# Kernel tuning notes

Hardware: AMD Instinct MI355X
Metric: run time of the kernel (lower is better)

Reference implementation:

```python
import jax, jax.numpy as jnp
import numpy as np

N = 10000
E = 160000
UNITS = 64
NUM_RBF = 32
CUTOFF = 1.0


def _xavier(k, shape):
    fan_out, fan_in = shape
    lim = float(np.sqrt(6.0 / (fan_in + fan_out)))
    return jax.random.uniform(k, shape, minval=-lim, maxval=lim, dtype=jnp.float32)


def setup_inputs() -> dict:
    key = jax.random.key(0)
    ks = jax.random.split(key, 16)
    inp = {
        "edge_index": jax.random.randint(ks[0], (2, E), 0, N),
        "edge_weight": jax.random.uniform(ks[1], (E,), dtype=jnp.float32),
        "edge_attr": jax.random.normal(ks[2], (E, NUM_RBF), dtype=jnp.float32),
        "X": jax.random.normal(ks[3], (N, UNITS, 3, 3), dtype=jnp.float32),
        # scalar MLP: num_rbf -> units -> 2*units -> 3*units
        "Ws0": _xavier(ks[4], (UNITS, NUM_RBF)), "bs0": jnp.zeros((UNITS,), jnp.float32),
        "Ws1": _xavier(ks[5], (2 * UNITS, UNITS)), "bs1": jnp.zeros((2 * UNITS,), jnp.float32),
        "Ws2": _xavier(ks[6], (3 * UNITS, 2 * UNITS)), "bs2": jnp.zeros((3 * UNITS,), jnp.float32),
    }
    for i in range(6):
        inp[f"Wt{i}"] = _xavier(ks[7 + i], (UNITS, UNITS))
    return inp


def cosine_cutoff(r, cutoff):
    return jnp.where(r < cutoff, 0.5 * (jnp.cos(jnp.pi * r / cutoff) + 1.0), 0.0)


def tensor_norm(X):
    # X: [N, units, 3, 3] -> [N, units]
    return jnp.sum(X * X, axis=(-2, -1))


def decompose_tensor(X):
    eye = jnp.eye(3, dtype=X.dtype)
    trace = jnp.trace(X, axis1=-2, axis2=-1)  # [N, units]
    I = (trace / 3.0)[..., None, None] * eye
    A = 0.5 * (X - jnp.swapaxes(X, -2, -1))
    S = 0.5 * (X + jnp.swapaxes(X, -2, -1)) - I
    return I, A, S


def channel_linear(T, W):
    # linear over the channel dim: [N, c, 3, 3] x [d, c] -> [N, d, 3, 3]
    return jnp.einsum('ncij,dc->ndij', T, W)


def reference(edge_index, edge_weight, edge_attr, X,
              Ws0, bs0, Ws1, bs1, Ws2, bs2,
              Wt0, Wt1, Wt2, Wt3, Wt4, Wt5):
    act = jax.nn.silu
    C = cosine_cutoff(edge_weight, CUTOFF)  # [E]
    h = act(edge_attr @ Ws0.T + bs0)
    h = act(h @ Ws1.T + bs1)
    h = act(h @ Ws2.T + bs2)  # [E, 3*units]
    ea = (h * C[:, None]).reshape(h.shape[0], UNITS, 3)  # [E, units, 3]

    X = X / (tensor_norm(X) + 1.0)[..., None, None]
    I, A, S = decompose_tensor(X)
    I = channel_linear(I, Wt0)
    A = channel_linear(A, Wt1)
    S = channel_linear(S, Wt2)
    Y = I + A + S

    src, dst = edge_index[0], edge_index[1]
    n = X.shape[0]
    # message = per-edge radial scaling of gathered node tensors; aggregate at src
    Im = jax.ops.segment_sum(ea[..., 0, None, None] * I[dst], src, num_segments=n)
    Am = jax.ops.segment_sum(ea[..., 1, None, None] * A[dst], src, num_segments=n)
    Sm = jax.ops.segment_sum(ea[..., 2, None, None] * S[dst], src, num_segments=n)
    msg = Im + Am + Sm

    # O(3): symmetrized product of batched 3x3 matmuls
    AB = jnp.matmul(msg, Y) + jnp.matmul(Y, msg)
    I2, A2, S2 = decompose_tensor(AB)
    normp1 = (tensor_norm(I2 + A2 + S2) + 1.0)[..., None, None]
    I2 = channel_linear(I2 / normp1, Wt3)
    A2 = channel_linear(A2 / normp1, Wt4)
    S2 = channel_linear(S2 / normp1, Wt5)
    dX = I2 + A2 + S2
    return X + dX + jnp.matmul(dX, dX)
```

## Files before the change

kernel.cpp:

```cpp
#include <hip/hip_runtime.h>
#include <math.h>

#define NN 10000
#define EE 160000

#define OFF_WTT 0
#define OFF_PK  24576
#define OFF_B2P 41984
#define OFF_IASH 42176
#define OFF_EAH 3242176
#define OFF_ATTRP 18602176
#define OFF_CP  21162176
#define OFF_INT 21322176

typedef __attribute__((ext_vector_type(8))) _Float16 h16x8;
typedef __attribute__((ext_vector_type(2))) __fp16 fp16x2_raw;
typedef __attribute__((ext_vector_type(4))) float f32x4;

__device__ __forceinline__ float silu_f(float x) {
    return x * __builtin_amdgcn_rcpf(1.0f + __expf(-x));
}
__device__ __forceinline__ unsigned int pkh(float a, float b) {
    union { fp16x2_raw h; unsigned int u; } cv;
    cv.h = __builtin_amdgcn_cvt_pkrtz(a, b);
    return cv.u;
}
__device__ __forceinline__ unsigned short f2h(float f) {
    union { _Float16 h; unsigned short u; } cv; cv.h = (_Float16)f; return cv.u;
}
__device__ __forceinline__ float h2f(unsigned short s) {
    union { unsigned short u; _Float16 h; } cv; cv.u = s; return (float)cv.h;
}
__device__ __forceinline__ float h2f_lo(unsigned int u) { return h2f((unsigned short)(u & 0xffffu)); }
__device__ __forceinline__ float h2f_hi(unsigned int u) { return h2f((unsigned short)(u >> 16)); }
__device__ __forceinline__ unsigned int bperm(int addr, unsigned int v) {
    return (unsigned int)__builtin_amdgcn_ds_bpermute(addr, (int)v);
}

__global__ void k_prep(const float* __restrict__ Wt0, const float* __restrict__ Wt1,
                       const float* __restrict__ Wt2, const float* __restrict__ Wt3,
                       const float* __restrict__ Wt4, const float* __restrict__ Wt5,
                       const float* __restrict__ Ws0, const float* __restrict__ Ws1,
                       const float* __restrict__ Ws2, const float* __restrict__ bs2,
                       const int* __restrict__ ei,
                       float* __restrict__ WtT, unsigned short* __restrict__ PK,
                       float* __restrict__ bs2p, int* __restrict__ counts) {
    int idx = blockIdx.x * 256 + threadIdx.x;
    if (idx < 24576) {
        int k = idx >> 12, r = idx & 4095;
        int c = r >> 6, d = r & 63;
        const float* W = (k == 0) ? Wt0 : (k == 1) ? Wt1 : (k == 2) ? Wt2
                       : (k == 3) ? Wt3 : (k == 4) ? Wt4 : Wt5;
        WtT[idx] = W[d * 64 + c];
    } else if (idx < 26624) {
        int q = idx - 24576;
        int ot = q >> 9, r = q & 511, lane = r >> 3, j = r & 7;
        int k = ((lane >> 4) * 8) + j, o = ot * 16 + (lane & 15);
        PK[q] = f2h(Ws0[o * 32 + k]);
    } else if (idx < 34816) {
        int q = idx - 24576;
        int i = q - 2048, ch = i >> 9, r = i & 511, lane = r >> 3, j = r & 7;
        int ot = ch >> 1, ks = ch & 1;
        int k = ks * 32 + (lane >> 4) * 8 + j, o = ot * 16 + (lane & 15);
        PK[q] = f2h(Ws1[o * 64 + k]);
    } else if (idx < 59392) {
        int q = idx - 24576;
        int i = q - 10240, ch = i >> 9, r = i & 511, lane = r >> 3, j = r & 7;
        int ot = ch >> 2, ks = ch & 3;
        int k = ks * 32 + (lane >> 4) * 8 + j;
        int op = ot * 16 + (lane & 15);
        int o = (op & 63) * 3 + (op >> 6);
        PK[q] = f2h(Ws2[o * 128 + k]);
    } else if (idx < 59584) {
        int op = idx - 59392;
        bs2p[op] = bs2[(op & 63) * 3 + (op >> 6)];
    } else if (idx < 59584 + EE) {
        int e = idx - 59584;
        atomicAdd(&counts[ei[e]], 1);
    }
}

__global__ __launch_bounds__(256) void k_scan(const int* __restrict__ counts,
                                              int* __restrict__ offsets) {
    __shared__ int sums[256];
    int t = threadIdx.x;
    int base = t * 40;
    int s = 0;
    if (base < NN) {
        const int4* p = (const int4*)(counts + base);
#pragma unroll
        for (int q = 0; q < 10; ++q) { int4 a = p[q]; s += a.x + a.y + a.z + a.w; }
    }
    sums[t] = s;
    __syncthreads();
    for (int off = 1; off < 256; off <<= 1) {
        int tmp = (t >= off) ? sums[t - off] : 0;
        __syncthreads();
        sums[t] += tmp;
        __syncthreads();
    }
    int run = sums[t] - s;
    if (base < NN) {
        const int4* p = (const int4*)(counts + base);
#pragma unroll
        for (int q = 0; q < 10; ++q) {
            int4 a = p[q];
            offsets[base + 4 * q + 0] = run; run += a.x;
            offsets[base + 4 * q + 1] = run; run += a.y;
            offsets[base + 4 * q + 2] = run; run += a.z;
            offsets[base + 4 * q + 3] = run; run += a.w;
        }
    }
    if (t == 255) offsets[NN] = run;
}

__global__ void k_fill(const int* __restrict__ ei, const int* __restrict__ offsets,
                       const float* __restrict__ attr, const float* __restrict__ ew,
                       int* __restrict__ cursor, int* __restrict__ dstp,
                       unsigned short* __restrict__ attrP, float* __restrict__ Cp) {
    int e = blockIdx.x * 256 + threadIdx.x;
    if (e < EE) {
        int s = ei[e];
        int pos = offsets[s] + atomicAdd(&cursor[s], 1);
        dstp[pos] = ei[EE + e];
        const float4* ap = (const float4*)(attr + (size_t)e * 32);
        unsigned int pk[16];
#pragma unroll
        for (int q = 0; q < 8; ++q) {
            float4 v = ap[q];
            pk[2 * q]     = pkh(v.x, v.y);
            pk[2 * q + 1] = pkh(v.z, v.w);
        }
        uint4* dst = (uint4*)(attrP + (size_t)pos * 32);
#pragma unroll
        for (int q = 0; q < 4; ++q)
            dst[q] = make_uint4(pk[4 * q], pk[4 * q + 1], pk[4 * q + 2], pk[4 * q + 3]);
        float rw = ew[e];
        Cp[pos] = (rw < 1.0f) ? 0.5f * (cosf(3.14159265358979f * rw) + 1.0f) : 0.0f;
    }
}

__global__ __launch_bounds__(256) void k_mlpnp(const unsigned short* __restrict__ attrP,
                                               const float* __restrict__ Cp,
                                               const unsigned short* __restrict__ PK,
                                               const float* __restrict__ bs0,
                                               const float* __restrict__ bs1,
                                               const float* __restrict__ bs2p,
                                               const float* __restrict__ X,
                                               const float* __restrict__ WtT,
                                               unsigned short* __restrict__ eah,
                                               unsigned int* __restrict__ IASu) {
    __shared__ float SH[4][1344];
    int t = threadIdx.x, w = t >> 6, l = t & 63;
    if (blockIdx.x < EE / 64) {
        int e = l & 15, lg = l >> 4;
        int pos = blockIdx.x * 64 + w * 16 + e;
        const h16x8* P1 = (const h16x8*)PK;
        const h16x8* P2 = (const h16x8*)(PK + 2048);
        const h16x8* P3 = (const h16x8*)(PK + 10240);
        union U8 { h16x8 h; unsigned int u[4]; uint4 v; };
        U8 B1;
        B1.v = *((const uint4*)(attrP + (size_t)pos * 32) + lg);
        float C = Cp[pos];
        int src0 = ((lg & 1) * 32 + e) * 4;
        int src1 = src0 + 64;
        bool hi = (lg >= 2);

        unsigned int h01[8], h23[8];
#pragma unroll
        for (int ot = 0; ot < 4; ++ot) {
            float4 bb = *(const float4*)&bs0[ot * 16 + lg * 4];
            f32x4 acc = {bb.x, bb.y, bb.z, bb.w};
            acc = __builtin_amdgcn_mfma_f32_16x16x32_f16(P1[ot * 64 + l], B1.h, acc, 0, 0, 0);
            h01[ot] = pkh(silu_f(acc[0]), silu_f(acc[1]));
            h23[ot] = pkh(silu_f(acc[2]), silu_f(acc[3]));
        }
        U8 B2a, B2b;
        {
            unsigned int a, b;
            a = bperm(src0, h01[0]); b = bperm(src0, h01[1]); B2a.u[0] = hi ? b : a;
            a = bperm(src0, h23[0]); b = bperm(src0, h23[1]); B2a.u[1] = hi ? b : a;
            a = bperm(src1, h01[0]); b = bperm(src1, h01[1]); B2a.u[2] = hi ? b : a;
            a = bperm(src1, h23[0]); b = bperm(src1, h23[1]); B2a.u[3] = hi ? b : a;
            a = bperm(src0, h01[2]); b = bperm(src0, h01[3]); B2b.u[0] = hi ? b : a;
            a = bperm(src0, h23[2]); b = bperm(src0, h23[3]); B2b.u[1] = hi ? b : a;
            a = bperm(src1, h01[2]); b = bperm(src1, h01[3]); B2b.u[2] = hi ? b : a;
            a = bperm(src1, h23[2]); b = bperm(src1, h23[3]); B2b.u[3] = hi ? b : a;
        }
#pragma unroll
        for (int ot = 0; ot < 8; ++ot) {
            float4 bb = *(const float4*)&bs1[ot * 16 + lg * 4];
            f32x4 acc = {bb.x, bb.y, bb.z, bb.w};
            acc = __builtin_amdgcn_mfma_f32_16x16x32_f16(P2[(ot * 2 + 0) * 64 + l], B2a.h, acc, 0, 0, 0);
            acc = __builtin_amdgcn_mfma_f32_16x16x32_f16(P2[(ot * 2 + 1) * 64 + l], B2b.h, acc, 0, 0, 0);
            h01[ot] = pkh(silu_f(acc[0]), silu_f(acc[1]));
            h23[ot] = pkh(silu_f(acc[2]), silu_f(acc[3]));
        }
        U8 B3[4];
#pragma unroll
        for (int ks = 0; ks < 4; ++ks) {
            unsigned int a, b;
            a = bperm(src0, h01[ks * 2]); b = bperm(src0, h01[ks * 2 + 1]); B3[ks].u[0] = hi ? b : a;
            a = bperm(src0, h23[ks * 2]); b = bperm(src0, h23[ks * 2 + 1]); B3[ks].u[1] = hi ? b : a;
            a = bperm(src1, h01[ks * 2]); b = bperm(src1, h01[ks * 2 + 1]); B3[ks].u[2] = hi ? b : a;
            a = bperm(src1, h23[ks * 2]); b = bperm(src1, h23[ks * 2 + 1]); B3[ks].u[3] = hi ? b : a;
        }
        size_t ebase = (size_t)pos * 192;
#pragma unroll
        for (int ot = 0; ot < 12; ++ot) {
            float4 bb = *(const float4*)&bs2p[ot * 16 + lg * 4];
            f32x4 acc = {bb.x, bb.y, bb.z, bb.w};
            acc = __builtin_amdgcn_mfma_f32_16x16x32_f16(P3[(ot * 4 + 0) * 64 + l], B3[0].h, acc, 0, 0, 0);
            acc = __builtin_amdgcn_mfma_f32_16x16x32_f16(P3[(ot * 4 + 1) * 64 + l], B3[1].h, acc, 0, 0, 0);
            acc = __builtin_amdgcn_mfma_f32_16x16x32_f16(P3[(ot * 4 + 2) * 64 + l], B3[2].h, acc, 0, 0, 0);
            acc = __builtin_amdgcn_mfma_f32_16x16x32_f16(P3[(ot * 4 + 3) * 64 + l], B3[3].h, acc, 0, 0, 0);
            unsigned int u01 = pkh(silu_f(acc[0]) * C, silu_f(acc[1]) * C);
            unsigned int u23 = pkh(silu_f(acc[2]) * C, silu_f(acc[3]) * C);
            *(uint2*)&eah[ebase + ot * 16 + lg * 4] = make_uint2(u01, u23);
        }
    } else {
        int c = l;
        int n = (blockIdx.x - EE / 64) * 4 + w;
        float* xs = SH[w];
        float (*L12)[12] = (float (*)[12])(xs + 576);
#pragma unroll
        for (int i = 0; i < 9; i++) xs[c + 64 * i] = X[(size_t)n * 576 + c + 64 * i];
        __builtin_amdgcn_wave_barrier();
        float x[9];
#pragma unroll
        for (int j = 0; j < 9; j++) x[j] = xs[c * 9 + j];
        float nrm = 0.f;
#pragma unroll
        for (int j = 0; j < 9; j++) nrm += x[j] * x[j];
        float inv = __builtin_amdgcn_rcpf(nrm + 1.0f);
#pragma unroll
        for (int j = 0; j < 9; j++) x[j] *= inv;
        float tr3 = (x[0] + x[4] + x[8]) * (1.0f / 3.0f);
        L12[c][0] = tr3;
        L12[c][1] = 0.5f * (x[1] - x[3]);
        L12[c][2] = 0.5f * (x[2] - x[6]);
        L12[c][3] = 0.5f * (x[5] - x[7]);
        L12[c][4] = x[0] - tr3;
        L12[c][5] = x[4] - tr3;
        L12[c][6] = 0.5f * (x[1] + x[3]);
        L12[c][7] = 0.5f * (x[2] + x[6]);
        L12[c][8] = 0.5f * (x[5] + x[7]);
        __builtin_amdgcn_wave_barrier();
        int d = c;
        const float* W0 = WtT;
        const float* W1 = WtT + 4096;
        const float* W2 = WtT + 8192;
        float aI = 0, aA0 = 0, aA1 = 0, aA2 = 0, aS0 = 0, aS1 = 0, aS2 = 0, aS3 = 0, aS4 = 0;
        for (int cc = 0; cc < 64; ++cc) {
            float w0 = W0[cc * 64 + d], w1 = W1[cc * 64 + d], w2 = W2[cc * 64 + d];
            float4 L0 = *(const float4*)&L12[cc][0];
            float4 L1 = *(const float4*)&L12[cc][4];
            float L8 = L12[cc][8];
            aI  += w0 * L0.x;
            aA0 += w1 * L0.y; aA1 += w1 * L0.z; aA2 += w1 * L0.w;
            aS0 += w2 * L1.x; aS1 += w2 * L1.y; aS2 += w2 * L1.z;
            aS3 += w2 * L1.w; aS4 += w2 * L8;
        }
        unsigned int* op = IASu + (size_t)n * 320 + d;
        op[0]   = pkh(aI, aA0);
        op[64]  = pkh(aA1, aA2);
        op[128] = pkh(aS0, aS1);
        op[192] = pkh(aS2, aS3);
        op[256] = pkh(aS4, 0.0f);
    }
}

__global__ __launch_bounds__(256) void k_aggout(const int* __restrict__ offsets,
                                                const int* __restrict__ dstp,
                                                const unsigned short* __restrict__ eah,
                                                const unsigned int* __restrict__ IASu,
                                                const float* __restrict__ X,
                                                const float* __restrict__ WtT,
                                                float* __restrict__ out) {
    int t = threadIdx.x, w = t >> 6, c = t & 63;
    int n = blockIdx.x * 4 + w;
    __shared__ float XS[4][576];
    __shared__ float LO[4][768];
    float* xs = XS[w];
    float* lo = LO[w];
#pragma unroll
    for (int i = 0; i < 9; i++) xs[c + 64 * i] = X[(size_t)n * 576 + c + 64 * i];

    int beg = offsets[n], end = offsets[n + 1];
    int dv = 0;
    { int idx = beg + c; if (idx < end) dv = dstp[idx]; }
    float m0 = 0, m1 = 0, m2 = 0, m3 = 0, m4 = 0, m5 = 0, m6 = 0, m7 = 0, m8 = 0;
    int i = beg;
    for (; i + 4 <= end; i += 4) {
        int q0 = i - beg;
        int d0 = (q0 < 64)     ? __shfl(dv, q0)     : dstp[i];
        int d1 = (q0 + 1 < 64) ? __shfl(dv, q0 + 1) : dstp[i + 1];
        int d2 = (q0 + 2 < 64) ? __shfl(dv, q0 + 2) : dstp[i + 2];
        int d3 = (q0 + 3 < 64) ? __shfl(dv, q0 + 3) : dstp[i + 3];
        int dd[4] = {d0, d1, d2, d3};
        float a[4][3];
        unsigned int u[4][5];
#pragma unroll
        for (int q = 0; q < 4; ++q) {
            const unsigned short* ep = eah + (size_t)(i + q) * 192;
            a[q][0] = h2f(ep[c]); a[q][1] = h2f(ep[64 + c]); a[q][2] = h2f(ep[128 + c]);
            const unsigned int* p = IASu + (size_t)dd[q] * 320 + c;
            u[q][0] = p[0]; u[q][1] = p[64]; u[q][2] = p[128]; u[q][3] = p[192]; u[q][4] = p[256];
        }
#pragma unroll
        for (int q = 0; q < 4; ++q) {
            m0 += a[q][0] * h2f_lo(u[q][0]); m1 += a[q][1] * h2f_hi(u[q][0]);
            m2 += a[q][1] * h2f_lo(u[q][1]); m3 += a[q][1] * h2f_hi(u[q][1]);
            m4 += a[q][2] * h2f_lo(u[q][2]); m5 += a[q][2] * h2f_hi(u[q][2]);
            m6 += a[q][2] * h2f_lo(u[q][3]); m7 += a[q][2] * h2f_hi(u[q][3]);
            m8 += a[q][2] * h2f_lo(u[q][4]);
        }
    }
    for (; i < end; ++i) {
        int q0 = i - beg;
        int dst = (q0 < 64) ? __shfl(dv, q0) : dstp[i];
        const unsigned short* ep = eah + (size_t)i * 192;
        float a0 = h2f(ep[c]), a1 = h2f(ep[64 + c]), a2 = h2f(ep[128 + c]);
        const unsigned int* p = IASu + (size_t)dst * 320 + c;
        unsigned int u0 = p[0], u1 = p[64], u2 = p[128], u3 = p[192], u4 = p[256];
        m0 += a0 * h2f_lo(u0); m1 += a1 * h2f_hi(u0);
        m2 += a1 * h2f_lo(u1); m3 += a1 * h2f_hi(u1);
        m4 += a2 * h2f_lo(u2); m5 += a2 * h2f_hi(u2);
        m6 += a2 * h2f_lo(u3); m7 += a2 * h2f_hi(u3);
        m8 += a2 * h2f_lo(u4);
    }
    const unsigned int* yp = IASu + (size_t)n * 320 + c;
    unsigned int y0 = yp[0], y1 = yp[64], y2 = yp[128], y3 = yp[192], y4 = yp[256];
    float yI = h2f_lo(y0), yA0 = h2f_hi(y0), yA1 = h2f_lo(y1), yA2 = h2f_hi(y1);
    float yS0 = h2f_lo(y2), yS1 = h2f_hi(y2), yS2 = h2f_lo(y3), yS3 = h2f_hi(y3);
    float yS4 = h2f_lo(y4);

    float M[3][3] = {
        { m0 + m4,   m1 + m6,  m2 + m7 },
        { -m1 + m6,  m0 + m5,  m3 + m8 },
        { -m2 + m7, -m3 + m8,  m0 - m4 - m5 } };
    float Y[3][3] = {
        { yI + yS0,   yA0 + yS2,  yA1 + yS3 },
        { -yA0 + yS2, yI + yS1,   yA2 + yS4 },
        { -yA1 + yS3, -yA2 + yS4, yI - yS0 - yS1 } };
    float AB[3][3];
#pragma unroll
    for (int ii = 0; ii < 3; ii++)
#pragma unroll
        for (int j = 0; j < 3; j++) {
            float s = 0.f;
#pragma unroll
            for (int k = 0; k < 3; k++) s += M[ii][k] * Y[k][j] + Y[ii][k] * M[k][j];
            AB[ii][j] = s;
        }
    float tr3 = (AB[0][0] + AB[1][1] + AB[2][2]) * (1.0f / 3.0f);
    float fro = 0.f;
#pragma unroll
    for (int ii = 0; ii < 3; ii++)
#pragma unroll
        for (int j = 0; j < 3; j++) fro += AB[ii][j] * AB[ii][j];
    float inv = __builtin_amdgcn_rcpf(fro + 1.0f);
    float (*L12)[12] = (float (*)[12])lo;
    L12[c][0] = tr3 * inv;
    L12[c][1] = 0.5f * (AB[0][1] - AB[1][0]) * inv;
    L12[c][2] = 0.5f * (AB[0][2] - AB[2][0]) * inv;
    L12[c][3] = 0.5f * (AB[1][2] - AB[2][1]) * inv;
    L12[c][4] = (AB[0][0] - tr3) * inv;
    L12[c][5] = (AB[1][1] - tr3) * inv;
    L12[c][6] = 0.5f * (AB[0][1] + AB[1][0]) * inv;
    L12[c][7] = 0.5f * (AB[0][2] + AB[2][0]) * inv;
    L12[c][8] = 0.5f * (AB[1][2] + AB[2][1]) * inv;
    __builtin_amdgcn_wave_barrier();
    int d = c;
    const float* W3 = WtT + 3 * 4096;
    const float* W4 = WtT + 4 * 4096;
    const float* W5 = WtT + 5 * 4096;
    float aI = 0, aA0 = 0, aA1 = 0, aA2 = 0, aS0 = 0, aS1 = 0, aS2 = 0, aS3 = 0, aS4 = 0;
    for (int cc = 0; cc < 64; ++cc) {
        float w3 = W3[cc * 64 + d], w4 = W4[cc * 64 + d], w5 = W5[cc * 64 + d];
        float4 L0 = *(const float4*)&L12[cc][0];
        float4 L1 = *(const float4*)&L12[cc][4];
        float L8 = L12[cc][8];
        aI  += w3 * L0.x;
        aA0 += w4 * L0.y; aA1 += w4 * L0.z; aA2 += w4 * L0.w;
        aS0 += w5 * L1.x; aS1 += w5 * L1.y; aS2 += w5 * L1.z;
        aS3 += w5 * L1.w; aS4 += w5 * L8;
    }
    float dX[3][3] = {
        { aI + aS0,   aA0 + aS2,  aA1 + aS3 },
        { -aA0 + aS2, aI + aS1,   aA2 + aS4 },
        { -aA1 + aS3, -aA2 + aS4, aI - aS0 - aS1 } };
    float D2[3][3];
#pragma unroll
    for (int ii = 0; ii < 3; ii++)
#pragma unroll
        for (int j = 0; j < 3; j++) {
            float s = 0.f;
#pragma unroll
            for (int k = 0; k < 3; k++) s += dX[ii][k] * dX[k][j];
            D2[ii][j] = s;
        }
    float x[9];
    __builtin_amdgcn_wave_barrier();
#pragma unroll
    for (int j = 0; j < 9; j++) x[j] = xs[d * 9 + j];
    float nrm = 0.f;
#pragma unroll
    for (int j = 0; j < 9; j++) nrm += x[j] * x[j];
    float xinv = __builtin_amdgcn_rcpf(nrm + 1.0f);
    __builtin_amdgcn_wave_barrier();
#pragma unroll
    for (int ii = 0; ii < 3; ii++)
#pragma unroll
        for (int j = 0; j < 3; j++)
            lo[d * 9 + ii * 3 + j] = x[ii * 3 + j] * xinv + dX[ii][j] + D2[ii][j];
    __builtin_amdgcn_wave_barrier();
#pragma unroll
    for (int ii = 0; ii < 9; ii++) out[(size_t)n * 576 + c + 64 * ii] = lo[c + 64 * ii];
}

extern "C" void kernel_launch(void* const* d_in, const int* in_sizes, int n_in,
                              void* d_out, int out_size, void* d_ws, size_t ws_size,
                              hipStream_t stream) {
    (void)in_sizes; (void)n_in; (void)out_size; (void)ws_size;
    const int* ei = (const int*)d_in[0];
    const float* ew = (const float*)d_in[1];
    const float* attr = (const float*)d_in[2];
    const float* X = (const float*)d_in[3];
    const float* Ws0 = (const float*)d_in[4];
    const float* bs0 = (const float*)d_in[5];
    const float* Ws1 = (const float*)d_in[6];
    const float* bs1 = (const float*)d_in[7];
    const float* Ws2 = (const float*)d_in[8];
    const float* bs2 = (const float*)d_in[9];
    const float* Wt0 = (const float*)d_in[10];
    const float* Wt1 = (const float*)d_in[11];
    const float* Wt2 = (const float*)d_in[12];
    const float* Wt3 = (const float*)d_in[13];
    const float* Wt4 = (const float*)d_in[14];
    const float* Wt5 = (const float*)d_in[15];
    float* ws = (float*)d_ws;
    int* ibase = (int*)(ws + OFF_INT);
    int* counts = ibase;
    int* cursor = ibase + NN;
    int* offsets = ibase + 2 * NN;
    int* dstp = ibase + 3 * NN + 1;
    unsigned short* PK = (unsigned short*)(ws + OFF_PK);
    unsigned int* IASu = (unsigned int*)(ws + OFF_IASH);
    unsigned short* eah = (unsigned short*)(ws + OFF_EAH);
    unsigned short* attrP = (unsigned short*)(ws + OFF_ATTRP);
    float* Cp = ws + OFF_CP;

    (void)hipMemsetAsync(counts, 0, 2 * NN * sizeof(int), stream);
    k_prep<<<(59584 + EE + 255) / 256, 256, 0, stream>>>(
        Wt0, Wt1, Wt2, Wt3, Wt4, Wt5, Ws0, Ws1, Ws2, bs2, ei,
        ws, PK, ws + OFF_B2P, counts);
    k_scan<<<1, 256, 0, stream>>>(counts, offsets);
    k_fill<<<(EE + 255) / 256, 256, 0, stream>>>(ei, offsets, attr, ew, cursor, dstp, attrP, Cp);
    k_mlpnp<<<EE / 64 + NN / 4, 256, 0, stream>>>(attrP, Cp, PK, bs0, bs1, ws + OFF_B2P,
                                                  X, ws, eah, IASu);
    k_aggout<<<NN / 4, 256, 0, stream>>>(offsets, dstp, eah, IASu, X, ws, (float*)d_out);
}
```

Baseline: 160.9 us.

## Regroup kernels: fuse node prep into fill, stage MLP weights in LDS, split aggregation

Node-side tensor preparation moves from the MLP kernel into the fill kernel. The edge MLP becomes its own kernel that stages the layer-2/3 fp16 weights (64KB) in shared memory and processes 256 edges per block across four iterations, instead of reading the weights from global memory for each 64-edge block. The aggregation kernel now assigns two waves per node, each summing half of the edge range, and merges the partial sums through shared memory. This aims to cut repeated weight fetches and shorten per-node serial loops, at the cost of 64KB LDS per block (lower occupancy), an extra block barrier, and dropping the shuffle-based dst prefetch.

New measurement: 165.1 us. +2.6%, slower.

```diff
diff --git a/kernel.cpp b/kernel.cpp
--- a/kernel.cpp
+++ b/kernel.cpp
@@ -114,12 +114,21 @@
     if (t == 255) offsets[NN] = run;
 }
 
-__global__ void k_fill(const int* __restrict__ ei, const int* __restrict__ offsets,
-                       const float* __restrict__ attr, const float* __restrict__ ew,
-                       int* __restrict__ cursor, int* __restrict__ dstp,
-                       unsigned short* __restrict__ attrP, float* __restrict__ Cp) {
-    int e = blockIdx.x * 256 + threadIdx.x;
-    if (e < EE) {
+__global__ __launch_bounds__(256) void k_fillnp(const int* __restrict__ ei,
+                                                const int* __restrict__ offsets,
+                                                const float* __restrict__ attr,
+                                                const float* __restrict__ ew,
+                                                const float* __restrict__ X,
+                                                const float* __restrict__ WtT,
+                                                int* __restrict__ cursor,
+                                                int* __restrict__ dstp,
+                                                unsigned short* __restrict__ attrP,
+                                                float* __restrict__ Cp,
+                                                unsigned int* __restrict__ IASu) {
+    __shared__ float SH[4][1344];
+    int t = threadIdx.x, w = t >> 6, l = t & 63;
+    if (blockIdx.x < 625) {
+        int e = blockIdx.x * 256 + t;
         int s = ei[e];
         int pos = offsets[s] + atomicAdd(&cursor[s], 1);
         dstp[pos] = ei[EE + e];
@@ -137,90 +146,9 @@
             dst[q] = make_uint4(pk[4 * q], pk[4 * q + 1], pk[4 * q + 2], pk[4 * q + 3]);
         float rw = ew[e];
         Cp[pos] = (rw < 1.0f) ? 0.5f * (cosf(3.14159265358979f * rw) + 1.0f) : 0.0f;
-    }
-}
-
-__global__ __launch_bounds__(256) void k_mlpnp(const unsigned short* __restrict__ attrP,
-                                               const float* __restrict__ Cp,
-                                               const unsigned short* __restrict__ PK,
-                                               const float* __restrict__ bs0,
-                                               const float* __restrict__ bs1,
-                                               const float* __restrict__ bs2p,
-                                               const float* __restrict__ X,
-                                               const float* __restrict__ WtT,
-                                               unsigned short* __restrict__ eah,
-                                               unsigned int* __restrict__ IASu) {
-    __shared__ float SH[4][1344];
-    int t = threadIdx.x, w = t >> 6, l = t & 63;
-    if (blockIdx.x < EE / 64) {
-        int e = l & 15, lg = l >> 4;
-        int pos = blockIdx.x * 64 + w * 16 + e;
-        const h16x8* P1 = (const h16x8*)PK;
-        const h16x8* P2 = (const h16x8*)(PK + 2048);
-        const h16x8* P3 = (const h16x8*)(PK + 10240);
-        union U8 { h16x8 h; unsigned int u[4]; uint4 v; };
-        U8 B1;
-        B1.v = *((const uint4*)(attrP + (size_t)pos * 32) + lg);
-        float C = Cp[pos];
-        int src0 = ((lg & 1) * 32 + e) * 4;
-        int src1 = src0 + 64;
-        bool hi = (lg >= 2);
-
-        unsigned int h01[8], h23[8];
-#pragma unroll
-        for (int ot = 0; ot < 4; ++ot) {
-            float4 bb = *(const float4*)&bs0[ot * 16 + lg * 4];
-            f32x4 acc = {bb.x, bb.y, bb.z, bb.w};
-            acc = __builtin_amdgcn_mfma_f32_16x16x32_f16(P1[ot * 64 + l], B1.h, acc, 0, 0, 0);
-            h01[ot] = pkh(silu_f(acc[0]), silu_f(acc[1]));
-            h23[ot] = pkh(silu_f(acc[2]), silu_f(acc[3]));
-        }
-        U8 B2a, B2b;
-        {
-            unsigned int a, b;
-            a = bperm(src0, h01[0]); b = bperm(src0, h01[1]); B2a.u[0] = hi ? b : a;
-            a = bperm(src0, h23[0]); b = bperm(src0, h23[1]); B2a.u[1] = hi ? b : a;
-            a = bperm(src1, h01[0]); b = bperm(src1, h01[1]); B2a.u[2] = hi ? b : a;
-            a = bperm(src1, h23[0]); b = bperm(src1, h23[1]); B2a.u[3] = hi ? b : a;
-            a = bperm(src0, h01[2]); b = bperm(src0, h01[3]); B2b.u[0] = hi ? b : a;
-            a = bperm(src0, h23[2]); b = bperm(src0, h23[3]); B2b.u[1] = hi ? b : a;
-            a = bperm(src1, h01[2]); b = bperm(src1, h01[3]); B2b.u[2] = hi ? b : a;
-            a = bperm(src1, h23[2]); b = bperm(src1, h23[3]); B2b.u[3] = hi ? b : a;
-        }
-#pragma unroll
-        for (int ot = 0; ot < 8; ++ot) {
-            float4 bb = *(const float4*)&bs1[ot * 16 + lg * 4];
-            f32x4 acc = {bb.x, bb.y, bb.z, bb.w};
-            acc = __builtin_amdgcn_mfma_f32_16x16x32_f16(P2[(ot * 2 + 0) * 64 + l], B2a.h, acc, 0, 0, 0);
-            acc = __builtin_amdgcn_mfma_f32_16x16x32_f16(P2[(ot * 2 + 1) * 64 + l], B2b.h, acc, 0, 0, 0);
-            h01[ot] = pkh(silu_f(acc[0]), silu_f(acc[1]));
-            h23[ot] = pkh(silu_f(acc[2]), silu_f(acc[3]));
-        }
-        U8 B3[4];
-#pragma unroll
-        for (int ks = 0; ks < 4; ++ks) {
-            unsigned int a, b;
-            a = bperm(src0, h01[ks * 2]); b = bperm(src0, h01[ks * 2 + 1]); B3[ks].u[0] = hi ? b : a;
-            a = bperm(src0, h23[ks * 2]); b = bperm(src0, h23[ks * 2 + 1]); B3[ks].u[1] = hi ? b : a;
-            a = bperm(src1, h01[ks * 2]); b = bperm(src1, h01[ks * 2 + 1]); B3[ks].u[2] = hi ? b : a;
-            a = bperm(src1, h23[ks * 2]); b = bperm(src1, h23[ks * 2 + 1]); B3[ks].u[3] = hi ? b : a;
-        }
-        size_t ebase = (size_t)pos * 192;
-#pragma unroll
-        for (int ot = 0; ot < 12; ++ot) {
-            float4 bb = *(const float4*)&bs2p[ot * 16 + lg * 4];
-            f32x4 acc = {bb.x, bb.y, bb.z, bb.w};
-            acc = __builtin_amdgcn_mfma_f32_16x16x32_f16(P3[(ot * 4 + 0) * 64 + l], B3[0].h, acc, 0, 0, 0);
-            acc = __builtin_amdgcn_mfma_f32_16x16x32_f16(P3[(ot * 4 + 1) * 64 + l], B3[1].h, acc, 0, 0, 0);
-            acc = __builtin_amdgcn_mfma_f32_16x16x32_f16(P3[(ot * 4 + 2) * 64 + l], B3[2].h, acc, 0, 0, 0);
-            acc = __builtin_amdgcn_mfma_f32_16x16x32_f16(P3[(ot * 4 + 3) * 64 + l], B3[3].h, acc, 0, 0, 0);
-            unsigned int u01 = pkh(silu_f(acc[0]) * C, silu_f(acc[1]) * C);
-            unsigned int u23 = pkh(silu_f(acc[2]) * C, silu_f(acc[3]) * C);
-            *(uint2*)&eah[ebase + ot * 16 + lg * 4] = make_uint2(u01, u23);
-        }
     } else {
         int c = l;
-        int n = (blockIdx.x - EE / 64) * 4 + w;
+        int n = (blockIdx.x - 625) * 4 + w;
         float* xs = SH[w];
         float (*L12)[12] = (float (*)[12])(xs + 576);
 #pragma unroll
@@ -270,6 +198,92 @@
     }
 }
 
+__global__ __launch_bounds__(256) void k_mlp(const unsigned short* __restrict__ attrP,
+                                             const float* __restrict__ Cp,
+                                             const unsigned short* __restrict__ PK,
+                                             const float* __restrict__ bs0,
+                                             const float* __restrict__ bs1,
+                                             const float* __restrict__ bs2p,
+                                             unsigned short* __restrict__ eah) {
+    __shared__ unsigned short WL[32768];
+    int t = threadIdx.x, w = t >> 6, l = t & 63;
+    {
+        const uint4* src = (const uint4*)(PK + 2048);
+        uint4* dst = (uint4*)WL;
+#pragma unroll
+        for (int q = 0; q < 16; ++q) dst[t + q * 256] = src[t + q * 256];
+    }
+    __syncthreads();
+    int e = l & 15, lg = l >> 4;
+    const h16x8* P1 = (const h16x8*)PK;
+    const h16x8* P2 = (const h16x8*)WL;
+    const h16x8* P3 = (const h16x8*)(WL + 8192);
+    int src0 = ((lg & 1) * 32 + e) * 4;
+    int src1 = src0 + 64;
+    bool hi = (lg >= 2);
+
+    for (int it = 0; it < 4; ++it) {
+        int pos = blockIdx.x * 256 + w * 64 + it * 16 + e;
+        union U8 { h16x8 h; unsigned int u[4]; uint4 v; };
+        U8 B1;
+        B1.v = *((const uint4*)(attrP + (size_t)pos * 32) + lg);
+        float C = Cp[pos];
+
+        unsigned int h01[8], h23[8];
+#pragma unroll
+        for (int ot = 0; ot < 4; ++ot) {
+            float4 bb = *(const float4*)&bs0[ot * 16 + lg * 4];
+            f32x4 acc = {bb.x, bb.y, bb.z, bb.w};
+            acc = __builtin_amdgcn_mfma_f32_16x16x32_f16(P1[ot * 64 + l], B1.h, acc, 0, 0, 0);
+            h01[ot] = pkh(silu_f(acc[0]), silu_f(acc[1]));
+            h23[ot] = pkh(silu_f(acc[2]), silu_f(acc[3]));
+        }
+        U8 B2a, B2b;
+        {
+            unsigned int a, b;
+            a = bperm(src0, h01[0]); b = bperm(src0, h01[1]); B2a.u[0] = hi ? b : a;
+            a = bperm(src0, h23[0]); b = bperm(src0, h23[1]); B2a.u[1] = hi ? b : a;
+            a = bperm(src1, h01[0]); b = bperm(src1, h01[1]); B2a.u[2] = hi ? b : a;
+            a = bperm(src1, h23[0]); b = bperm(src1, h23[1]); B2a.u[3] = hi ? b : a;
+            a = bperm(src0, h01[2]); b = bperm(src0, h01[3]); B2b.u[0] = hi ? b : a;
+            a = bperm(src0, h23[2]); b = bperm(src0, h23[3]); B2b.u[1] = hi ? b : a;
+            a = bperm(src1, h01[2]); b = bperm(src1, h01[3]); B2b.u[2] = hi ? b : a;
+            a = bperm(src1, h23[2]); b = bperm(src1, h23[3]); B2b.u[3] = hi ? b : a;
+        }
+#pragma unroll
+        for (int ot = 0; ot < 8; ++ot) {
+            float4 bb = *(const float4*)&bs1[ot * 16 + lg * 4];
+            f32x4 acc = {bb.x, bb.y, bb.z, bb.w};
+            acc = __builtin_amdgcn_mfma_f32_16x16x32_f16(P2[(ot * 2 + 0) * 64 + l], B2a.h, acc, 0, 0, 0);
+            acc = __builtin_amdgcn_mfma_f32_16x16x32_f16(P2[(ot * 2 + 1) * 64 + l], B2b.h, acc, 0, 0, 0);
+            h01[ot] = pkh(silu_f(acc[0]), silu_f(acc[1]));
+            h23[ot] = pkh(silu_f(acc[2]), silu_f(acc[3]));
+        }
+        U8 B3[4];
+#pragma unroll
+        for (int ks = 0; ks < 4; ++ks) {
+            unsigned int a, b;
+            a = bperm(src0, h01[ks * 2]); b = bperm(src0, h01[ks * 2 + 1]); B3[ks].u[0] = hi ? b : a;
+            a = bperm(src0, h23[ks * 2]); b = bperm(src0, h23[ks * 2 + 1]); B3[ks].u[1] = hi ? b : a;
+            a = bperm(src1, h01[ks * 2]); b = bperm(src1, h01[ks * 2 + 1]); B3[ks].u[2] = hi ? b : a;
+            a = bperm(src1, h23[ks * 2]); b = bperm(src1, h23[ks * 2 + 1]); B3[ks].u[3] = hi ? b : a;
+        }
+        size_t ebase = (size_t)pos * 192;
+#pragma unroll
+        for (int ot = 0; ot < 12; ++ot) {
+            float4 bb = *(const float4*)&bs2p[ot * 16 + lg * 4];
+            f32x4 acc = {bb.x, bb.y, bb.z, bb.w};
+            acc = __builtin_amdgcn_mfma_f32_16x16x32_f16(P3[(ot * 4 + 0) * 64 + l], B3[0].h, acc, 0, 0, 0);
+            acc = __builtin_amdgcn_mfma_f32_16x16x32_f16(P3[(ot * 4 + 1) * 64 + l], B3[1].h, acc, 0, 0, 0);
+            acc = __builtin_amdgcn_mfma_f32_16x16x32_f16(P3[(ot * 4 + 2) * 64 + l], B3[2].h, acc, 0, 0, 0);
+            acc = __builtin_amdgcn_mfma_f32_16x16x32_f16(P3[(ot * 4 + 3) * 64 + l], B3[3].h, acc, 0, 0, 0);
+            unsigned int u01 = pkh(silu_f(acc[0]) * C, silu_f(acc[1]) * C);
+            unsigned int u23 = pkh(silu_f(acc[2]) * C, silu_f(acc[3]) * C);
+            *(uint2*)&eah[ebase + ot * 16 + lg * 4] = make_uint2(u01, u23);
+        }
+    }
+}
+
 __global__ __launch_bounds__(256) void k_aggout(const int* __restrict__ offsets,
                                                 const int* __restrict__ dstp,
                                                 const unsigned short* __restrict__ eah,
@@ -278,33 +292,38 @@
                                                 const float* __restrict__ WtT,
                                                 float* __restrict__ out) {
     int t = threadIdx.x, w = t >> 6, c = t & 63;
-    int n = blockIdx.x * 4 + w;
-    __shared__ float XS[4][576];
-    __shared__ float LO[4][768];
-    float* xs = XS[w];
-    float* lo = LO[w];
-#pragma unroll
-    for (int i = 0; i < 9; i++) xs[c + 64 * i] = X[(size_t)n * 576 + c + 64 * i];
+    int nw = w >> 1, half = w & 1;
+    int n = blockIdx.x * 2 + nw;
+    __shared__ float PS[2][9][64];
+    __shared__ float XS[2][576];
+    __shared__ float LO[2][768];
+    float* xs = XS[nw];
+    float* lo = LO[nw];
+    if (half == 0) {
+#pragma unroll
+        for (int i = 0; i < 5; i++) xs[c + 64 * i] = X[(size_t)n * 576 + c + 64 * i];
+    } else {
+#pragma unroll
+        for (int i = 5; i < 9; i++) xs[c + 64 * i] = X[(size_t)n * 576 + c + 64 * i];
+    }
 
     int beg = offsets[n], end = offsets[n + 1];
-    int dv = 0;
-    { int idx = beg + c; if (idx < end) dv = dstp[idx]; }
+    int deg = end - beg;
+    int mid = beg + (((deg / 2) + 3) & ~3);
+    if (mid > end) mid = end;
+    int i0 = half ? mid : beg;
+    int i1 = half ? end : mid;
+
     float m0 = 0, m1 = 0, m2 = 0, m3 = 0, m4 = 0, m5 = 0, m6 = 0, m7 = 0, m8 = 0;
-    int i = beg;
-    for (; i + 4 <= end; i += 4) {
-        int q0 = i - beg;
-        int d0 = (q0 < 64)     ? __shfl(dv, q0)     : dstp[i];
-        int d1 = (q0 + 1 < 64) ? __shfl(dv, q0 + 1) : dstp[i + 1];
-        int d2 = (q0 + 2 < 64) ? __shfl(dv, q0 + 2) : dstp[i + 2];
-        int d3 = (q0 + 3 < 64) ? __shfl(dv, q0 + 3) : dstp[i + 3];
-        int dd[4] = {d0, d1, d2, d3};
+    int i = i0;
+    for (; i + 4 <= i1; i += 4) {
         float a[4][3];
         unsigned int u[4][5];
 #pragma unroll
         for (int q = 0; q < 4; ++q) {
             const unsigned short* ep = eah + (size_t)(i + q) * 192;
             a[q][0] = h2f(ep[c]); a[q][1] = h2f(ep[64 + c]); a[q][2] = h2f(ep[128 + c]);
-            const unsigned int* p = IASu + (size_t)dd[q] * 320 + c;
+            const unsigned int* p = IASu + (size_t)dstp[i + q] * 320 + c;
             u[q][0] = p[0]; u[q][1] = p[64]; u[q][2] = p[128]; u[q][3] = p[192]; u[q][4] = p[256];
         }
 #pragma unroll
@@ -316,12 +335,10 @@
             m8 += a[q][2] * h2f_lo(u[q][4]);
         }
     }
-    for (; i < end; ++i) {
-        int q0 = i - beg;
-        int dst = (q0 < 64) ? __shfl(dv, q0) : dstp[i];
+    for (; i < i1; ++i) {
         const unsigned short* ep = eah + (size_t)i * 192;
         float a0 = h2f(ep[c]), a1 = h2f(ep[64 + c]), a2 = h2f(ep[128 + c]);
-        const unsigned int* p = IASu + (size_t)dst * 320 + c;
+        const unsigned int* p = IASu + (size_t)dstp[i] * 320 + c;
         unsigned int u0 = p[0], u1 = p[64], u2 = p[128], u3 = p[192], u4 = p[256];
         m0 += a0 * h2f_lo(u0); m1 += a1 * h2f_hi(u0);
         m2 += a1 * h2f_lo(u1); m3 += a1 * h2f_hi(u1);
@@ -329,6 +346,17 @@
         m6 += a2 * h2f_lo(u3); m7 += a2 * h2f_hi(u3);
         m8 += a2 * h2f_lo(u4);
     }
+    if (half == 1) {
+        PS[nw][0][c] = m0; PS[nw][1][c] = m1; PS[nw][2][c] = m2;
+        PS[nw][3][c] = m3; PS[nw][4][c] = m4; PS[nw][5][c] = m5;
+        PS[nw][6][c] = m6; PS[nw][7][c] = m7; PS[nw][8][c] = m8;
+    }
+    __syncthreads();
+    if (half == 1) return;
+    m0 += PS[nw][0][c]; m1 += PS[nw][1][c]; m2 += PS[nw][2][c];
+    m3 += PS[nw][3][c]; m4 += PS[nw][4][c]; m5 += PS[nw][5][c];
+    m6 += PS[nw][6][c]; m7 += PS[nw][7][c]; m8 += PS[nw][8][c];
+
     const unsigned int* yp = IASu + (size_t)n * 320 + c;
     unsigned int y0 = yp[0], y1 = yp[64], y2 = yp[128], y3 = yp[192], y4 = yp[256];
     float yI = h2f_lo(y0), yA0 = h2f_hi(y0), yA1 = h2f_lo(y1), yA2 = h2f_hi(y1);
@@ -456,8 +484,8 @@
         Wt0, Wt1, Wt2, Wt3, Wt4, Wt5, Ws0, Ws1, Ws2, bs2, ei,
         ws, PK, ws + OFF_B2P, counts);
     k_scan<<<1, 256, 0, stream>>>(counts, offsets);
-    k_fill<<<(EE + 255) / 256, 256, 0, stream>>>(ei, offsets, attr, ew, cursor, dstp, attrP, Cp);
-    k_mlpnp<<<EE / 64 + NN / 4, 256, 0, stream>>>(attrP, Cp, PK, bs0, bs1, ws + OFF_B2P,
-                                                  X, ws, eah, IASu);
-    k_aggout<<<NN / 4, 256, 0, stream>>>(offsets, dstp, eah, IASu, X, ws, (float*)d_out);
-}
+    k_fillnp<<<625 + NN / 4, 256, 0, stream>>>(ei, offsets, attr, ew, X, ws,
+                                               cursor, dstp, attrP, Cp, IASu);
+    k_mlp<<<625, 256, 0, stream>>>(attrP, Cp, PK, bs0, bs1, ws + OFF_B2P, eah);
+    k_aggout<<<NN / 2, 256, 0, stream>>>(offsets, dstp, eah, IASu, X, ws, (float*)d_out);
+}
```
